# Optimization experiments

Hardware: AMD Instinct MI355X
Metric: run time of the kernel (lower is better)

The kernel has to match this reference:

```python
import jax, jax.numpy as jnp
import numpy as np

B, T, D, L = 128, 32, 512, 2


def setup_inputs() -> dict:
    key = jax.random.key(0)
    ks = jax.random.split(key, 8)
    s = 0.02
    inp = {
        "cognition_features": jax.random.normal(ks[0], (B, T, D), dtype=jnp.float32),
        # per-layer stacked params (leading dim L)
        "Wq": s * jax.random.normal(ks[1], (L, D, D), dtype=jnp.float32),
        "bq": jnp.zeros((L, D), jnp.float32),
        "Wk": s * jax.random.normal(ks[2], (L, D, D), dtype=jnp.float32),
        "bk": jnp.zeros((L, D), jnp.float32),
        "Wv": s * jax.random.normal(ks[3], (L, D, D), dtype=jnp.float32),
        "bv": jnp.zeros((L, D), jnp.float32),
        "ln1_g": jnp.ones((L, D), jnp.float32),
        "ln1_b": jnp.zeros((L, D), jnp.float32),
        "W1": s * jax.random.normal(ks[4], (L, 4 * D, D), dtype=jnp.float32),
        "b1": jnp.zeros((L, 4 * D), jnp.float32),
        "W2": s * jax.random.normal(ks[5], (L, D, 4 * D), dtype=jnp.float32),
        "b2": jnp.zeros((L, D), jnp.float32),
        "ln2_g": jnp.ones((L, D), jnp.float32),
        "ln2_b": jnp.zeros((L, D), jnp.float32),
        # gate mlp (random instead of zeros/ones init to avoid degenerate constant gate)
        "Ws": s * jax.random.normal(ks[6], (D, 2 * D), dtype=jnp.float32),
        "bs": jnp.zeros((D,), jnp.float32),
    }
    return inp


def _ln(x, g, b, eps=1e-5):
    mu = jnp.mean(x, axis=-1, keepdims=True)
    var = jnp.mean((x - mu) ** 2, axis=-1, keepdims=True)
    return (x - mu) * jax.lax.rsqrt(var + eps) * g + b


def reference(cognition_features, Wq, bq, Wk, bk, Wv, bv, ln1_g, ln1_b,
              W1, b1, W2, b2, ln2_g, ln2_b, Ws, bs):
    b_, t_, d_ = cognition_features.shape
    L_ = Wq.shape[0]
    # memory bank entries are detached originals of earlier batch items
    mem = jax.lax.stop_gradient(cognition_features).reshape(b_ * t_, d_)
    mem_item = jnp.arange(b_ * t_) // t_
    visible = mem_item[None, :] < jnp.arange(b_)[:, None]  # [B, B*T]
    neg = jnp.asarray(-1e9, cognition_features.dtype)
    scale = 1.0 / jnp.sqrt(jnp.asarray(d_, cognition_features.dtype))

    x = cognition_features
    for l in range(L_):
        q = x @ Wq[l].T + bq[l]                      # [B,T,D]
        k = mem @ Wk[l].T + bk[l]                    # [B*T,D]
        v = mem @ Wv[l].T + bv[l]
        s = jnp.einsum('btd,md->btm', q, k) * scale  # [B,T,B*T]
        s = jnp.where(visible[:, None, :], s, neg)
        a = jax.nn.softmax(s, axis=-1)
        attn = jnp.einsum('btm,md->btd', a, v)
        x = _ln(x + attn, ln1_g[l], ln1_b[l])
        h = jax.nn.gelu(x @ W1[l].T + b1[l], approximate=False)
        x = _ln(x + h @ W2[l].T + b2[l], ln2_g[l], ln2_b[l])

    # item 0 has an empty bank: blocks are skipped, attn_out = query
    attn_out = jnp.where((jnp.arange(b_) == 0)[:, None, None], cognition_features, x)
    cat = jnp.concatenate([cognition_features, attn_out], axis=-1)
    g = jax.nn.sigmoid(cat @ Ws.T + bs)
    return g * cognition_features + (1.0 - g) * attn_out
```

## Files before the change

kernel.cpp:

```cpp
#include <hip/hip_runtime.h>
#include <cmath>


#define ROWS 4096
#define DIM  512

typedef __bf16 bf16x8 __attribute__((ext_vector_type(8)));
typedef float  f32x4  __attribute__((ext_vector_type(4)));
typedef unsigned short u16;
typedef u16 u16x4 __attribute__((ext_vector_type(4)));
typedef u16 u16x8 __attribute__((ext_vector_type(8)));

#define RD ((size_t)ROWS * DIM)
#define BUFU 12288

__device__ __forceinline__ u16 f2bf(float x) {
    union { float f; unsigned u; } c; c.f = x;
    const unsigned r = (c.u + 0x7FFFu + ((c.u >> 16) & 1u)) >> 16;
    return (u16)r;
}

__device__ __forceinline__ void gload16(const void* g, void* l) {
    __builtin_amdgcn_global_load_lds(
        (const __attribute__((address_space(1))) void*)g,
        (__attribute__((address_space(3))) void*)l, 16, 0, 0);
}

__device__ __forceinline__ float gelu_f(float v) {
    return 0.5f * v * (1.0f + erff(v * 0.70710678118654752f));
}

template<int EPI>
__device__ __forceinline__ void mgemm_body(
    const u16* __restrict__ A, int lda,
    const u16* __restrict__ B, int ldb,
    const float* __restrict__ bias,
    void* __restrict__ C, int ldc,
    int kBeg, int kEnd, float scale, int m0, int n0, u16* smem,
    float* __restrict__ sums)
{
    const int tid  = threadIdx.x;
    const int lane = tid & 63;
    const int w    = tid >> 6;
    const int wr   = (w >> 1) << 5;
    const int wc   = (w & 1) << 6;

    f32x4 acc[2][4];
    #pragma unroll
    for (int i = 0; i < 2; ++i)
        #pragma unroll
        for (int j = 0; j < 4; ++j)
            acc[i][j] = (f32x4){0.f, 0.f, 0.f, 0.f};

    const u16* gpA[2]; int loA[2];
    #pragma unroll
    for (int q = 0; q < 2; ++q) {
        const int c = (q << 2) + w;
        const int s = (c << 6) + lane;
        const int row = s >> 3, sub = (s & 7) ^ (row & 7);
        gpA[q] = A + (size_t)(m0 + row) * lda + (sub << 3) + kBeg;
        loA[q] = c << 9;
    }
    const u16* gpB[4]; int loB[4];
    #pragma unroll
    for (int q = 0; q < 4; ++q) {
        const int c = ((q + 2) << 2) + w - 8;
        const int s = (c << 6) + lane;
        const int row = s >> 3, sub = (s & 7) ^ (row & 7);
        gpB[q] = B + (size_t)(n0 + row) * ldb + (sub << 3) + kBeg;
        loB[q] = 4096 + (c << 9);
    }

    const int l15 = lane & 15, kg = lane >> 4;
    int aoff[2][2], boff[4][2];
    #pragma unroll
    for (int i = 0; i < 2; ++i)
        #pragma unroll
        for (int h = 0; h < 2; ++h) {
            const int r = wr + (i << 4) + l15;
            const int sub = ((h << 2) + kg) ^ (r & 7);
            aoff[i][h] = ((r << 3) + sub) << 3;
        }
    #pragma unroll
    for (int j = 0; j < 4; ++j)
        #pragma unroll
        for (int h = 0; h < 2; ++h) {
            const int r = wc + (j << 4) + l15;
            const int sub = ((h << 2) + kg) ^ (r & 7);
            boff[j][h] = 4096 + (((r << 3) + sub) << 3);
        }

    const int nt = (kEnd - kBeg) >> 6;

    auto STAGE = [&](int t, int bsel) {
        u16* base = smem + bsel * BUFU;
        const int ko = t << 6;
        gload16(gpA[0] + ko, base + loA[0]);
        gload16(gpA[1] + ko, base + loA[1]);
        gload16(gpB[0] + ko, base + loB[0]);
        gload16(gpB[1] + ko, base + loB[1]);
        gload16(gpB[2] + ko, base + loB[2]);
        gload16(gpB[3] + ko, base + loB[3]);
    };

    if (nt > 0) {
        STAGE(0, 0);
        if (nt > 1) STAGE(1, 1);
        for (int t = 0; t < nt; ++t) {
            if (t + 1 < nt) asm volatile("s_waitcnt vmcnt(6)" ::: "memory");
            else            asm volatile("s_waitcnt vmcnt(0)" ::: "memory");
            __builtin_amdgcn_s_barrier();
            asm volatile("" ::: "memory");

            const u16* buf = smem + (t & 1) * BUFU;
            bf16x8 a_[2][2], b_[4][2];
            #pragma unroll
            for (int i = 0; i < 2; ++i)
                #pragma unroll
                for (int h = 0; h < 2; ++h)
                    a_[i][h] = *reinterpret_cast<const bf16x8*>(&buf[aoff[i][h]]);
            #pragma unroll
            for (int j = 0; j < 4; ++j)
                #pragma unroll
                for (int h = 0; h < 2; ++h)
                    b_[j][h] = *reinterpret_cast<const bf16x8*>(&buf[boff[j][h]]);

            asm volatile("s_waitcnt lgkmcnt(0)" ::: "memory");
            __builtin_amdgcn_s_barrier();
            asm volatile("" ::: "memory");

            if (t + 2 < nt) STAGE(t + 2, t & 1);

            __builtin_amdgcn_s_setprio(1);
            #pragma unroll
            for (int h = 0; h < 2; ++h)
                #pragma unroll
                for (int i = 0; i < 2; ++i)
                    #pragma unroll
                    for (int j = 0; j < 4; ++j) {
                        if (EPI == 4)
                            acc[i][j] = __builtin_amdgcn_mfma_f32_16x16x32_bf16(
                                a_[i][h], b_[j][h], acc[i][j], 0, 0, 0);
                        else
                            acc[i][j] = __builtin_amdgcn_mfma_f32_16x16x32_bf16(
                                b_[j][h], a_[i][h], acc[i][j], 0, 0, 0);
                    }
            __builtin_amdgcn_s_setprio(0);
        }
    }

    const int lq = lane >> 4;
    if (EPI == 4) {
        #pragma unroll
        for (int j = 0; j < 4; ++j) {
            const int col = n0 + wc + (j << 4) + l15;
            const float bj = bias[col];
            #pragma unroll
            for (int i = 0; i < 2; ++i) {
                const int row0 = m0 + wr + (i << 4) + (lq << 2);
                u16x4 pk;
                #pragma unroll
                for (int r = 0; r < 4; ++r) pk[r] = f2bf(acc[i][j][r] + bj);
                *reinterpret_cast<u16x4*>(&((u16*)C)[(size_t)col * ldc + row0]) = pk;
            }
        }
    } else if (EPI == 5) {
        float rs0 = 0.f, rs1 = 0.f;
        #pragma unroll
        for (int j = 0; j < 4; ++j) {
            const int col0 = n0 + wc + (j << 4) + (lq << 2);
            #pragma unroll
            for (int i = 0; i < 2; ++i) {
                const int row = m0 + wr + (i << 4) + l15;
                const int lim = (row >> 5) << 5;
                f32x4 v = acc[i][j];
                u16x4 pk;
                float rsl = 0.f;
                #pragma unroll
                for (int r = 0; r < 4; ++r) {
                    const float e = (col0 + r < lim) ? __expf(v[r] * scale) : 0.f;
                    rsl += e;
                    pk[r] = f2bf(e);
                }
                if (i == 0) rs0 += rsl; else rs1 += rsl;
                *reinterpret_cast<u16x4*>(&((u16*)C)[(size_t)row * ldc + col0]) = pk;
            }
        }
        rs0 += __shfl_xor(rs0, 16); rs0 += __shfl_xor(rs0, 32);
        rs1 += __shfl_xor(rs1, 16); rs1 += __shfl_xor(rs1, 32);
        if (lq == 0) {
            atomicAdd(&sums[m0 + wr + l15], rs0);
            atomicAdd(&sums[m0 + wr + 16 + l15], rs1);
        }
    } else {
        #pragma unroll
        for (int j = 0; j < 4; ++j) {
            const int col0 = n0 + wc + (j << 4) + (lq << 2);
            float4 bj = {0.f, 0.f, 0.f, 0.f};
            if (EPI != 0) bj = *reinterpret_cast<const float4*>(&bias[col0]);
            #pragma unroll
            for (int i = 0; i < 2; ++i) {
                const int row = m0 + wr + (i << 4) + l15;
                f32x4 v = acc[i][j];
                if (EPI == 0) {
                    v[0] *= scale; v[1] *= scale; v[2] *= scale; v[3] *= scale;
                    *reinterpret_cast<f32x4*>(&((float*)C)[(size_t)row * ldc + col0]) = v;
                } else if (EPI == 1) {
                    v[0] += bj.x; v[1] += bj.y; v[2] += bj.z; v[3] += bj.w;
                    *reinterpret_cast<f32x4*>(&((float*)C)[(size_t)row * ldc + col0]) = v;
                } else {
                    v[0] += bj.x; v[1] += bj.y; v[2] += bj.z; v[3] += bj.w;
                    if (EPI == 3) {
                        v[0] = gelu_f(v[0]); v[1] = gelu_f(v[1]);
                        v[2] = gelu_f(v[2]); v[3] = gelu_f(v[3]);
                    }
                    u16x4 pk = {f2bf(v[0]), f2bf(v[1]), f2bf(v[2]), f2bf(v[3])};
                    *reinterpret_cast<u16x4*>(&((u16*)C)[(size_t)row * ldc + col0]) = pk;
                }
            }
        }
    }
}

template<int EPI>
__global__ __launch_bounds__(256, 3) void mgemm(
    const u16* __restrict__ A, int lda, const u16* __restrict__ B, int ldb,
    const float* __restrict__ bias, void* __restrict__ C, int ldc, int K, float scale)
{
    const int m0 = blockIdx.x << 6;
    const int n0 = blockIdx.y << 7;
    __shared__ u16 smem[2 * BUFU];
    mgemm_body<EPI>(A, lda, B, ldb, bias, C, ldc, 0, K, scale, m0, n0, smem, nullptr);
}

__device__ __forceinline__ int tri_pref(int b) {
    const int h = b >> 1;
    return (b & 1) ? (h + 1) * (h + 1) : h * (h + 1);
}
__global__ __launch_bounds__(256, 3) void mgemm_tri(
    const u16* __restrict__ A, const u16* __restrict__ B,
    u16* __restrict__ P, float* __restrict__ sums, float scale)
{
    const int z = blockIdx.x;
    int bx = 2 * (int)sqrtf((float)z);
    while (tri_pref(bx + 1) <= z) ++bx;
    while (tri_pref(bx) > z) --bx;
    const int by = z - tri_pref(bx);
    __shared__ u16 smem[2 * BUFU];
    mgemm_body<5>(A, 512, B, 512, nullptr, P, 4096, 0, 512, scale,
                  bx << 6, by << 7, smem, sums);
}

template<bool AVK>
__global__ __launch_bounds__(256, 3) void mgemm_pk(
    const u16* __restrict__ A, int lda, const u16* __restrict__ B, int ldb,
    float* __restrict__ Cpart, int K, int chunk)
{
    const int m0 = blockIdx.x << 6;
    const int n0 = blockIdx.y << 7;
    const int z  = blockIdx.z;
    const int Klim = AVK ? (m0 + 64) : K;
    const int ch = AVK ? ((((Klim >> 2) + 63) >> 6) << 6) : chunk;
    int kBeg = z * ch; if (kBeg > Klim) kBeg = Klim;
    int kEnd = kBeg + ch; if (kEnd > Klim) kEnd = Klim;
    __shared__ u16 smem[2 * BUFU];
    mgemm_body<0>(A, lda, B, ldb, nullptr, Cpart + (size_t)z * RD, 512,
                  kBeg, kEnd, 1.f, m0, n0, smem, nullptr);
}

__global__ __launch_bounds__(256, 3) void mgemm_part(
    const u16* __restrict__ A, int lda, const u16* __restrict__ B, int ldb,
    float* __restrict__ Cpart)
{
    const int m0 = blockIdx.x << 6;
    const int n0 = blockIdx.y << 7;
    __shared__ u16 smem[2 * BUFU];
    mgemm_body<0>(A, lda, B, ldb, nullptr, Cpart, 512,
                  0, 512, 1.f, m0, n0, smem, nullptr);
}

__global__ __launch_bounds__(256, 3) void qkv_gemm(
    const u16* __restrict__ xa, const u16* __restrict__ cfb,
    const u16* __restrict__ Wqb, const u16* __restrict__ Wkb, const u16* __restrict__ Wvb,
    const float* __restrict__ bq, const float* __restrict__ bk, const float* __restrict__ bv,
    u16* __restrict__ q, u16* __restrict__ k, u16* __restrict__ vT)
{
    __shared__ u16 smem[2 * BUFU];
    const int m0 = blockIdx.x << 6;
    const int which = blockIdx.y >> 2;
    const int n0 = (blockIdx.y & 3) << 7;
    if (which == 0)
        mgemm_body<2>(xa,  512, Wqb, 512, bq, q,  512,  0, 512, 1.f, m0, n0, smem, nullptr);
    else if (which == 1)
        mgemm_body<2>(cfb, 512, Wkb, 512, bk, k,  512,  0, 512, 1.f, m0, n0, smem, nullptr);
    else
        mgemm_body<4>(cfb, 512, Wvb, 512, bv, vT, 4096, 0, 512, 1.f, m0, n0, smem, nullptr);
}

template<int NS, bool HASB, bool DIV>
__global__ __launch_bounds__(256) void ln_res_ps(
    const float* __restrict__ Xin, const float* __restrict__ part,
    const float* __restrict__ bias, const float* __restrict__ sums,
    const float* __restrict__ gamma, const float* __restrict__ beta,
    float* __restrict__ Xout, u16* __restrict__ Xbf)
{
    const int row  = blockIdx.x * 4 + (threadIdx.x >> 6);
    const int lane = threadIdx.x & 63;
    const float* xr = Xin + (size_t)row * DIM;
    const int d0 = lane << 3;
    const float inv = DIV ? (1.0f / fmaxf(sums[row], 1e-30f)) : 1.0f;

    const float4 x0 = *reinterpret_cast<const float4*>(&xr[d0]);
    const float4 x1 = *reinterpret_cast<const float4*>(&xr[d0 + 4]);
    float a[8] = {0.f, 0.f, 0.f, 0.f, 0.f, 0.f, 0.f, 0.f};
    #pragma unroll
    for (int s = 0; s < NS; ++s) {
        const float* pr = part + (size_t)s * RD + (size_t)row * DIM + d0;
        const float4 p0 = *reinterpret_cast<const float4*>(pr);
        const float4 p1 = *reinterpret_cast<const float4*>(pr + 4);
        a[0] += p0.x; a[1] += p0.y; a[2] += p0.z; a[3] += p0.w;
        a[4] += p1.x; a[5] += p1.y; a[6] += p1.z; a[7] += p1.w;
    }
    float v[8] = {x0.x, x0.y, x0.z, x0.w, x1.x, x1.y, x1.z, x1.w};
    #pragma unroll
    for (int i = 0; i < 8; ++i) v[i] += a[i] * inv;
    if (HASB) {
        const float4 b0 = *reinterpret_cast<const float4*>(&bias[d0]);
        const float4 b1 = *reinterpret_cast<const float4*>(&bias[d0 + 4]);
        v[0] += b0.x; v[1] += b0.y; v[2] += b0.z; v[3] += b0.w;
        v[4] += b1.x; v[5] += b1.y; v[6] += b1.z; v[7] += b1.w;
    }

    float sm = 0.f;
    #pragma unroll
    for (int i = 0; i < 8; ++i) sm += v[i];
    #pragma unroll
    for (int off = 32; off; off >>= 1) sm += __shfl_xor(sm, off);
    const float mu = sm * (1.0f / 512.0f);

    float qs = 0.f;
    #pragma unroll
    for (int i = 0; i < 8; ++i) { const float d = v[i] - mu; qs += d * d; }
    #pragma unroll
    for (int off = 32; off; off >>= 1) qs += __shfl_xor(qs, off);
    const float rs = rsqrtf(qs * (1.0f / 512.0f) + 1e-5f);

    const float4 g0 = *reinterpret_cast<const float4*>(&gamma[d0]);
    const float4 g1 = *reinterpret_cast<const float4*>(&gamma[d0 + 4]);
    const float4 b0 = *reinterpret_cast<const float4*>(&beta[d0]);
    const float4 b1 = *reinterpret_cast<const float4*>(&beta[d0 + 4]);
    float o[8];
    o[0] = (v[0] - mu) * rs * g0.x + b0.x;
    o[1] = (v[1] - mu) * rs * g0.y + b0.y;
    o[2] = (v[2] - mu) * rs * g0.z + b0.z;
    o[3] = (v[3] - mu) * rs * g0.w + b0.w;
    o[4] = (v[4] - mu) * rs * g1.x + b1.x;
    o[5] = (v[5] - mu) * rs * g1.y + b1.y;
    o[6] = (v[6] - mu) * rs * g1.z + b1.z;
    o[7] = (v[7] - mu) * rs * g1.w + b1.w;

    float4 f0 = {o[0], o[1], o[2], o[3]}, f1 = {o[4], o[5], o[6], o[7]};
    *reinterpret_cast<float4*>(&Xout[(size_t)row * DIM + d0])     = f0;
    *reinterpret_cast<float4*>(&Xout[(size_t)row * DIM + d0 + 4]) = f1;
    u16x8 ob;
    #pragma unroll
    for (int i = 0; i < 8; ++i) ob[i] = f2bf(o[i]);
    *reinterpret_cast<u16x8*>(&Xbf[(size_t)row * DIM + d0]) = ob;
}

struct ConvArgs {
    const float* src[7];
    u16* dst[7];
    int start[8];
};

__global__ __launch_bounds__(256) void conv_all(ConvArgs a)
{
    const int b = blockIdx.x;
    int seg = 0;
    #pragma unroll
    for (int i = 1; i < 7; ++i) seg += (a.start[i] <= b) ? 1 : 0;
    const int i = ((b - a.start[seg]) * 256 + threadIdx.x) << 3;
    const float* s = a.src[seg];
    const float4 lo = *reinterpret_cast<const float4*>(&s[i]);
    const float4 hi = *reinterpret_cast<const float4*>(&s[i + 4]);
    u16x8 o = {f2bf(lo.x), f2bf(lo.y), f2bf(lo.z), f2bf(lo.w),
               f2bf(hi.x), f2bf(hi.y), f2bf(hi.z), f2bf(hi.w)};
    *reinterpret_cast<u16x8*>(&a.dst[seg][i]) = o;
}

__global__ __launch_bounds__(256) void zero_sums(float4* __restrict__ s)
{
    s[blockIdx.x * 256 + threadIdx.x] = (float4){0.f, 0.f, 0.f, 0.f};
}

__global__ __launch_bounds__(256) void fix_x0(u16* __restrict__ xbf,
                                              const u16* __restrict__ cfb)
{
    const int i = (blockIdx.x * 256 + threadIdx.x) << 3;
    *reinterpret_cast<u16x8*>(&xbf[i]) =
        *reinterpret_cast<const u16x8*>(&cfb[i]);
}

__global__ __launch_bounds__(256) void final_gate_ps(
    float4* __restrict__ out, const float4* __restrict__ cf,
    const float4* __restrict__ x, const float* __restrict__ part,
    const float* __restrict__ bias)
{
    const int idx = blockIdx.x * 256 + threadIdx.x;
    const int row = idx >> 7;
    const int c4  = idx & 127;
    const float4 zc = cf[idx];
    const float4 p0 = reinterpret_cast<const float4*>(part)[idx];
    const float4 p1 = reinterpret_cast<const float4*>(part + RD)[idx];
    const float4 bb = *reinterpret_cast<const float4*>(&bias[c4 << 2]);
    const float4 za = (row < 32) ? zc : x[idx];
    float4 o;
    { const float g = 1.0f / (1.0f + expf(-(p0.x + p1.x + bb.x))); o.x = g * zc.x + (1.0f - g) * za.x; }
    { const float g = 1.0f / (1.0f + expf(-(p0.y + p1.y + bb.y))); o.y = g * zc.y + (1.0f - g) * za.y; }
    { const float g = 1.0f / (1.0f + expf(-(p0.z + p1.z + bb.z))); o.z = g * zc.z + (1.0f - g) * za.z; }
    { const float g = 1.0f / (1.0f + expf(-(p0.w + p1.w + bb.w))); o.w = g * zc.w + (1.0f - g) * za.w; }
    out[idx] = o;
}

extern "C" void kernel_launch(void* const* d_in, const int* in_sizes, int n_in,
                              void* d_out, int out_size, void* d_ws, size_t ws_size,
                              hipStream_t stream)
{
    const float* cf   = (const float*)d_in[0];
    const float* Wq   = (const float*)d_in[1];
    const float* bq   = (const float*)d_in[2];
    const float* Wk   = (const float*)d_in[3];
    const float* bk   = (const float*)d_in[4];
    const float* Wv   = (const float*)d_in[5];
    const float* bv   = (const float*)d_in[6];
    const float* ln1g = (const float*)d_in[7];
    const float* ln1b = (const float*)d_in[8];
    const float* W1   = (const float*)d_in[9];
    const float* b1   = (const float*)d_in[10];
    const float* W2   = (const float*)d_in[11];
    const float* b2   = (const float*)d_in[12];
    const float* ln2g = (const float*)d_in[13];
    const float* ln2b = (const float*)d_in[14];
    const float* Wsg  = (const float*)d_in[15];
    const float* bsg  = (const float*)d_in[16];
    float* out = (float*)d_out;

    float* ws   = (float*)d_ws;
    float* x    = ws;
    float* sums = ws + RD;
    float* part = ws + 2 * RD;
    u16*  pbf  = (u16*)(ws + 10 * RD);
    u16*  hbf  = (u16*)(ws + 10 * RD);
    u16*  bfb  = (u16*)(ws + 14 * RD);
    u16* cfb = bfb;
    u16* xbf = bfb + RD;
    u16* qbf = bfb + 2 * RD;
    u16* kbf = bfb + 3 * RD;
    u16* vTb = bfb + 4 * RD;
    u16* Wqb = bfb + 5 * RD;
    u16* Wkb = Wqb + 524288;
    u16* Wvb = Wkb + 524288;
    u16* W1b = Wvb + 524288;
    u16* W2b = W1b + 2097152;
    u16* Wsb = W2b + 2097152;

    const float scale = 0.044194173824159216f;

    ConvArgs ca;
    ca.src[0] = cf;  ca.dst[0] = cfb;
    ca.src[1] = Wq;  ca.dst[1] = Wqb;
    ca.src[2] = Wk;  ca.dst[2] = Wkb;
    ca.src[3] = Wv;  ca.dst[3] = Wvb;
    ca.src[4] = W1;  ca.dst[4] = W1b;
    ca.src[5] = W2;  ca.dst[5] = W2b;
    ca.src[6] = Wsg; ca.dst[6] = Wsb;
    ca.start[0] = 0;    ca.start[1] = 1024; ca.start[2] = 1280;
    ca.start[3] = 1536; ca.start[4] = 1792; ca.start[5] = 2816;
    ca.start[6] = 3840; ca.start[7] = 4096;
    conv_all<<<4096, 256, 0, stream>>>(ca);

    for (int l = 0; l < 2; ++l) {
        const u16* xa = (l == 0) ? cfb : xbf;
        zero_sums<<<4, 256, 0, stream>>>((float4*)sums);
        qkv_gemm<<<dim3(64, 12), 256, 0, stream>>>(
            xa, cfb, Wqb + l * 262144, Wkb + l * 262144, Wvb + l * 262144,
            bq + l * 512, bk + l * 512, bv + l * 512, qbf, kbf, vTb);
        mgemm_tri<<<1056, 256, 0, stream>>>(qbf, kbf, pbf, sums, scale);
        mgemm_pk<true><<<dim3(64, 4, 4), 256, 0, stream>>>(
            pbf, 4096, vTb, 4096, part, 4096, 0);
        ln_res_ps<4, false, true><<<1024, 256, 0, stream>>>(
            (l == 0) ? cf : x, part, nullptr, sums,
            ln1g + l * 512, ln1b + l * 512, x, xbf);
        mgemm<3><<<dim3(64, 16), 256, 0, stream>>>(
            xbf, 512, W1b + l * 1048576, 512, b1 + l * 2048, hbf, 2048, 512, 1.f);
        mgemm_pk<false><<<dim3(64, 4, 4), 256, 0, stream>>>(
            hbf, 2048, W2b + l * 1048576, 2048, part, 2048, 512);
        ln_res_ps<4, true, false><<<1024, 256, 0, stream>>>(
            x, part, b2 + l * 512, nullptr,
            ln2g + l * 512, ln2b + l * 512, x, xbf);
    }

    fix_x0<<<8, 256, 0, stream>>>(xbf, cfb);
    mgemm_part<<<dim3(64, 4), 256, 0, stream>>>(cfb, 512, Wsb,       1024, part);
    mgemm_part<<<dim3(64, 4), 256, 0, stream>>>(xbf, 512, Wsb + 512, 1024, part + RD);
    final_gate_ps<<<2048, 256, 0, stream>>>((float4*)out, (const float4*)cf,
                                            (const float4*)x, part, bsg);
}
```

Measured before the change: 251.5 us.

## Store split-K partials in bf16, merge gate GEMMs, drop extra launches

Split-K partial outputs of the attention-V and W2 GEMMs, plus the gate GEMM outputs, are now written as bf16 instead of fp32. This halves the partial-buffer traffic read back by the layernorm and final-gate kernels. The two gate GEMMs are merged into one launch, with row selection of the query source for item 0 done inside the GEMM, which removes the fix_x0 copy kernel. The softmax sums buffer is zeroed once and then reset inside the layernorm kernel, removing a per-layer launch. Rounding partial sums to bf16 lowers accuracy.

```diff
diff --git a/kernel.cpp b/kernel.cpp
--- a/kernel.cpp
+++ b/kernel.cpp
@@ -19,6 +19,10 @@
     const unsigned r = (c.u + 0x7FFFu + ((c.u >> 16) & 1u)) >> 16;
     return (u16)r;
 }
+__device__ __forceinline__ float bf2f(u16 h) {
+    union { unsigned u; float f; } c; c.u = ((unsigned)h) << 16;
+    return c.f;
+}
 
 __device__ __forceinline__ void gload16(const void* g, void* l) {
     __builtin_amdgcn_global_load_lds(
@@ -30,14 +34,14 @@
     return 0.5f * v * (1.0f + erff(v * 0.70710678118654752f));
 }
 
-template<int EPI>
+template<int EPI, bool MIX>
 __device__ __forceinline__ void mgemm_body(
     const u16* __restrict__ A, int lda,
     const u16* __restrict__ B, int ldb,
     const float* __restrict__ bias,
     void* __restrict__ C, int ldc,
     int kBeg, int kEnd, float scale, int m0, int n0, u16* smem,
-    float* __restrict__ sums)
+    float* __restrict__ sums, const u16* __restrict__ Amix)
 {
     const int tid  = threadIdx.x;
     const int lane = tid & 63;
@@ -58,7 +62,9 @@
         const int c = (q << 2) + w;
         const int s = (c << 6) + lane;
         const int row = s >> 3, sub = (s & 7) ^ (row & 7);
-        gpA[q] = A + (size_t)(m0 + row) * lda + (sub << 3) + kBeg;
+        const u16* Abase = A;
+        if (MIX) Abase = ((m0 + row) < 32) ? Amix : A;
+        gpA[q] = Abase + (size_t)(m0 + row) * lda + (sub << 3) + kBeg;
         loA[q] = c << 9;
     }
     const u16* gpB[4]; int loB[4];
@@ -197,7 +203,8 @@
         for (int j = 0; j < 4; ++j) {
             const int col0 = n0 + wc + (j << 4) + (lq << 2);
             float4 bj = {0.f, 0.f, 0.f, 0.f};
-            if (EPI != 0) bj = *reinterpret_cast<const float4*>(&bias[col0]);
+            if (EPI == 1 || EPI == 2 || EPI == 3)
+                bj = *reinterpret_cast<const float4*>(&bias[col0]);
             #pragma unroll
             for (int i = 0; i < 2; ++i) {
                 const int row = m0 + wr + (i << 4) + l15;
@@ -208,6 +215,10 @@
                 } else if (EPI == 1) {
                     v[0] += bj.x; v[1] += bj.y; v[2] += bj.z; v[3] += bj.w;
                     *reinterpret_cast<f32x4*>(&((float*)C)[(size_t)row * ldc + col0]) = v;
+                } else if (EPI == 6) {
+                    u16x4 pk = {f2bf(v[0] * scale), f2bf(v[1] * scale),
+                                f2bf(v[2] * scale), f2bf(v[3] * scale)};
+                    *reinterpret_cast<u16x4*>(&((u16*)C)[(size_t)row * ldc + col0]) = pk;
                 } else {
                     v[0] += bj.x; v[1] += bj.y; v[2] += bj.z; v[3] += bj.w;
                     if (EPI == 3) {
@@ -230,7 +241,8 @@
     const int m0 = blockIdx.x << 6;
     const int n0 = blockIdx.y << 7;
     __shared__ u16 smem[2 * BUFU];
-    mgemm_body<EPI>(A, lda, B, ldb, bias, C, ldc, 0, K, scale, m0, n0, smem, nullptr);
+    mgemm_body<EPI, false>(A, lda, B, ldb, bias, C, ldc, 0, K, scale, m0, n0,
+                           smem, nullptr, nullptr);
 }
 
 __device__ __forceinline__ int tri_pref(int b) {
@@ -247,14 +259,14 @@
     while (tri_pref(bx) > z) --bx;
     const int by = z - tri_pref(bx);
     __shared__ u16 smem[2 * BUFU];
-    mgemm_body<5>(A, 512, B, 512, nullptr, P, 4096, 0, 512, scale,
-                  bx << 6, by << 7, smem, sums);
+    mgemm_body<5, false>(A, 512, B, 512, nullptr, P, 4096, 0, 512, scale,
+                         bx << 6, by << 7, smem, sums, nullptr);
 }
 
 template<bool AVK>
 __global__ __launch_bounds__(256, 3) void mgemm_pk(
     const u16* __restrict__ A, int lda, const u16* __restrict__ B, int ldb,
-    float* __restrict__ Cpart, int K, int chunk)
+    u16* __restrict__ Cpart, int K, int chunk)
 {
     const int m0 = blockIdx.x << 6;
     const int n0 = blockIdx.y << 7;
@@ -264,19 +276,24 @@
     int kBeg = z * ch; if (kBeg > Klim) kBeg = Klim;
     int kEnd = kBeg + ch; if (kEnd > Klim) kEnd = Klim;
     __shared__ u16 smem[2 * BUFU];
-    mgemm_body<0>(A, lda, B, ldb, nullptr, Cpart + (size_t)z * RD, 512,
-                  kBeg, kEnd, 1.f, m0, n0, smem, nullptr);
-}
-
-__global__ __launch_bounds__(256, 3) void mgemm_part(
-    const u16* __restrict__ A, int lda, const u16* __restrict__ B, int ldb,
-    float* __restrict__ Cpart)
+    mgemm_body<6, false>(A, lda, B, ldb, nullptr, Cpart + (size_t)z * RD, 512,
+                         kBeg, kEnd, 1.f, m0, n0, smem, nullptr, nullptr);
+}
+
+__global__ __launch_bounds__(256, 3) void g_gate(
+    const u16* __restrict__ cfb, const u16* __restrict__ xbf,
+    const u16* __restrict__ Wsb, u16* __restrict__ Cpart)
 {
     const int m0 = blockIdx.x << 6;
     const int n0 = blockIdx.y << 7;
+    const int z  = blockIdx.z;
     __shared__ u16 smem[2 * BUFU];
-    mgemm_body<0>(A, lda, B, ldb, nullptr, Cpart, 512,
-                  0, 512, 1.f, m0, n0, smem, nullptr);
+    if (z == 0)
+        mgemm_body<6, false>(cfb, 512, Wsb, 1024, nullptr, Cpart, 512,
+                             0, 512, 1.f, m0, n0, smem, nullptr, nullptr);
+    else
+        mgemm_body<6, true>(xbf, 512, Wsb + 512, 1024, nullptr, Cpart + RD, 512,
+                            0, 512, 1.f, m0, n0, smem, nullptr, cfb);
 }
 
 __global__ __launch_bounds__(256, 3) void qkv_gemm(
@@ -290,17 +307,20 @@
     const int which = blockIdx.y >> 2;
     const int n0 = (blockIdx.y & 3) << 7;
     if (which == 0)
-        mgemm_body<2>(xa,  512, Wqb, 512, bq, q,  512,  0, 512, 1.f, m0, n0, smem, nullptr);
+        mgemm_body<2, false>(xa,  512, Wqb, 512, bq, q,  512,  0, 512, 1.f,
+                             m0, n0, smem, nullptr, nullptr);
     else if (which == 1)
-        mgemm_body<2>(cfb, 512, Wkb, 512, bk, k,  512,  0, 512, 1.f, m0, n0, smem, nullptr);
+        mgemm_body<2, false>(cfb, 512, Wkb, 512, bk, k,  512,  0, 512, 1.f,
+                             m0, n0, smem, nullptr, nullptr);
     else
-        mgemm_body<4>(cfb, 512, Wvb, 512, bv, vT, 4096, 0, 512, 1.f, m0, n0, smem, nullptr);
+        mgemm_body<4, false>(cfb, 512, Wvb, 512, bv, vT, 4096, 0, 512, 1.f,
+                             m0, n0, smem, nullptr, nullptr);
 }
 
 template<int NS, bool HASB, bool DIV>
 __global__ __launch_bounds__(256) void ln_res_ps(
-    const float* __restrict__ Xin, const float* __restrict__ part,
-    const float* __restrict__ bias, const float* __restrict__ sums,
+    const float* __restrict__ Xin, const u16* __restrict__ partb,
+    const float* __restrict__ bias, float* __restrict__ sums,
     const float* __restrict__ gamma, const float* __restrict__ beta,
     float* __restrict__ Xout, u16* __restrict__ Xbf)
 {
@@ -309,17 +329,17 @@
     const float* xr = Xin + (size_t)row * DIM;
     const int d0 = lane << 3;
     const float inv = DIV ? (1.0f / fmaxf(sums[row], 1e-30f)) : 1.0f;
+    if (DIV && lane == 0) sums[row] = 0.f;
 
     const float4 x0 = *reinterpret_cast<const float4*>(&xr[d0]);
     const float4 x1 = *reinterpret_cast<const float4*>(&xr[d0 + 4]);
     float a[8] = {0.f, 0.f, 0.f, 0.f, 0.f, 0.f, 0.f, 0.f};
     #pragma unroll
     for (int s = 0; s < NS; ++s) {
-        const float* pr = part + (size_t)s * RD + (size_t)row * DIM + d0;
-        const float4 p0 = *reinterpret_cast<const float4*>(pr);
-        const float4 p1 = *reinterpret_cast<const float4*>(pr + 4);
-        a[0] += p0.x; a[1] += p0.y; a[2] += p0.z; a[3] += p0.w;
-        a[4] += p1.x; a[5] += p1.y; a[6] += p1.z; a[7] += p1.w;
+        const u16* pr = partb + (size_t)s * RD + (size_t)row * DIM + d0;
+        const u16x8 pv = *reinterpret_cast<const u16x8*>(pr);
+        #pragma unroll
+        for (int i = 0; i < 8; ++i) a[i] += bf2f(pv[i]);
     }
     float v[8] = {x0.x, x0.y, x0.z, x0.w, x1.x, x1.y, x1.z, x1.w};
     #pragma unroll
@@ -394,32 +414,24 @@
     s[blockIdx.x * 256 + threadIdx.x] = (float4){0.f, 0.f, 0.f, 0.f};
 }
 
-__global__ __launch_bounds__(256) void fix_x0(u16* __restrict__ xbf,
-                                              const u16* __restrict__ cfb)
-{
-    const int i = (blockIdx.x * 256 + threadIdx.x) << 3;
-    *reinterpret_cast<u16x8*>(&xbf[i]) =
-        *reinterpret_cast<const u16x8*>(&cfb[i]);
-}
-
 __global__ __launch_bounds__(256) void final_gate_ps(
     float4* __restrict__ out, const float4* __restrict__ cf,
-    const float4* __restrict__ x, const float* __restrict__ part,
+    const float4* __restrict__ x, const u16* __restrict__ partb,
     const float* __restrict__ bias)
 {
     const int idx = blockIdx.x * 256 + threadIdx.x;
     const int row = idx >> 7;
     const int c4  = idx & 127;
     const float4 zc = cf[idx];
-    const float4 p0 = reinterpret_cast<const float4*>(part)[idx];
-    const float4 p1 = reinterpret_cast<const float4*>(part + RD)[idx];
+    const u16x4 q0 = *reinterpret_cast<const u16x4*>(&partb[(size_t)idx * 4]);
+    const u16x4 q1 = *reinterpret_cast<const u16x4*>(&partb[RD + (size_t)idx * 4]);
     const float4 bb = *reinterpret_cast<const float4*>(&bias[c4 << 2]);
     const float4 za = (row < 32) ? zc : x[idx];
     float4 o;
-    { const float g = 1.0f / (1.0f + expf(-(p0.x + p1.x + bb.x))); o.x = g * zc.x + (1.0f - g) * za.x; }
-    { const float g = 1.0f / (1.0f + expf(-(p0.y + p1.y + bb.y))); o.y = g * zc.y + (1.0f - g) * za.y; }
-    { const float g = 1.0f / (1.0f + expf(-(p0.z + p1.z + bb.z))); o.z = g * zc.z + (1.0f - g) * za.z; }
-    { const float g = 1.0f / (1.0f + expf(-(p0.w + p1.w + bb.w))); o.w = g * zc.w + (1.0f - g) * za.w; }
+    { const float g = 1.0f / (1.0f + expf(-(bf2f(q0[0]) + bf2f(q1[0]) + bb.x))); o.x = g * zc.x + (1.0f - g) * za.x; }
+    { const float g = 1.0f / (1.0f + expf(-(bf2f(q0[1]) + bf2f(q1[1]) + bb.y))); o.y = g * zc.y + (1.0f - g) * za.y; }
+    { const float g = 1.0f / (1.0f + expf(-(bf2f(q0[2]) + bf2f(q1[2]) + bb.z))); o.z = g * zc.z + (1.0f - g) * za.z; }
+    { const float g = 1.0f / (1.0f + expf(-(bf2f(q0[3]) + bf2f(q1[3]) + bb.w))); o.w = g * zc.w + (1.0f - g) * za.w; }
     out[idx] = o;
 }
 
@@ -449,7 +461,7 @@
     float* ws   = (float*)d_ws;
     float* x    = ws;
     float* sums = ws + RD;
-    float* part = ws + 2 * RD;
+    u16*  partb = (u16*)(ws + 2 * RD);
     u16*  pbf  = (u16*)(ws + 10 * RD);
     u16*  hbf  = (u16*)(ws + 10 * RD);
     u16*  bfb  = (u16*)(ws + 14 * RD);
@@ -479,31 +491,29 @@
     ca.start[3] = 1536; ca.start[4] = 1792; ca.start[5] = 2816;
     ca.start[6] = 3840; ca.start[7] = 4096;
     conv_all<<<4096, 256, 0, stream>>>(ca);
+    zero_sums<<<4, 256, 0, stream>>>((float4*)sums);
 
     for (int l = 0; l < 2; ++l) {
         const u16* xa = (l == 0) ? cfb : xbf;
-        zero_sums<<<4, 256, 0, stream>>>((float4*)sums);
         qkv_gemm<<<dim3(64, 12), 256, 0, stream>>>(
             xa, cfb, Wqb + l * 262144, Wkb + l * 262144, Wvb + l * 262144,
             bq + l * 512, bk + l * 512, bv + l * 512, qbf, kbf, vTb);
         mgemm_tri<<<1056, 256, 0, stream>>>(qbf, kbf, pbf, sums, scale);
         mgemm_pk<true><<<dim3(64, 4, 4), 256, 0, stream>>>(
-            pbf, 4096, vTb, 4096, part, 4096, 0);
+            pbf, 4096, vTb, 4096, partb, 4096, 0);
         ln_res_ps<4, false, true><<<1024, 256, 0, stream>>>(
-            (l == 0) ? cf : x, part, nullptr, sums,
+            (l == 0) ? cf : x, partb, nullptr, sums,
             ln1g + l * 512, ln1b + l * 512, x, xbf);
         mgemm<3><<<dim3(64, 16), 256, 0, stream>>>(
             xbf, 512, W1b + l * 1048576, 512, b1 + l * 2048, hbf, 2048, 512, 1.f);
         mgemm_pk<false><<<dim3(64, 4, 4), 256, 0, stream>>>(
-            hbf, 2048, W2b + l * 1048576, 2048, part, 2048, 512);
+            hbf, 2048, W2b + l * 1048576, 2048, partb, 2048, 512);
         ln_res_ps<4, true, false><<<1024, 256, 0, stream>>>(
-            x, part, b2 + l * 512, nullptr,
+            x, partb, b2 + l * 512, nullptr,
             ln2g + l * 512, ln2b + l * 512, x, xbf);
     }
 
-    fix_x0<<<8, 256, 0, stream>>>(xbf, cfb);
-    mgemm_part<<<dim3(64, 4), 256, 0, stream>>>(cfb, 512, Wsb,       1024, part);
-    mgemm_part<<<dim3(64, 4), 256, 0, stream>>>(xbf, 512, Wsb + 512, 1024, part + RD);
+    g_gate<<<dim3(64, 4, 2), 256, 0, stream>>>(cfb, xbf, Wsb, partb);
     final_gate_ps<<<2048, 256, 0, stream>>>((float4*)out, (const float4*)cf,
-                                            (const float4*)x, part, bsg);
-}
+                                            (const float4*)x, partb, bsg);
+}
```

Result: faster. 234.1 us (-6.9%).
